# Performance work log

Hardware: AMD Instinct MI355X
Metric: run time of the kernel (lower is better)

## Reference

```python
import jax, jax.numpy as jnp
import numpy as np

P, B, H, IN, L = 64, 256, 512, 2, 2


def setup_inputs() -> dict:
    key = jax.random.key(0)
    ks = jax.random.split(key, 16)
    s = 1.0 / np.sqrt(H)
    inp = {
        'input_traces': jax.random.normal(ks[0], (B, P, IN), jnp.float32),
        'h0': jax.random.normal(ks[1], (P, L, B, H), jnp.float32) * 0.1,
        'c0': jax.random.normal(ks[2], (P, L, B, H), jnp.float32) * 0.1,
        # layer 0 LSTM params (PyTorch layout: [4H, in] with gate order i,f,g,o)
        'w_ih0': jax.random.uniform(ks[3], (4 * H, IN), jnp.float32, -s, s),
        'w_hh0': jax.random.uniform(ks[4], (4 * H, H), jnp.float32, -s, s),
        'b_ih0': jax.random.uniform(ks[5], (4 * H,), jnp.float32, -s, s),
        'b_hh0': jax.random.uniform(ks[6], (4 * H,), jnp.float32, -s, s),
        # layer 1 LSTM params
        'w_ih1': jax.random.uniform(ks[7], (4 * H, H), jnp.float32, -s, s),
        'w_hh1': jax.random.uniform(ks[8], (4 * H, H), jnp.float32, -s, s),
        'b_ih1': jax.random.uniform(ks[9], (4 * H,), jnp.float32, -s, s),
        'b_hh1': jax.random.uniform(ks[10], (4 * H,), jnp.float32, -s, s),
    }
    return inp


def _lstm_forward(input_traces, h0, c0, params):
    # Fuse pedestrian and batch dims into one big batch PB = P*B; the original
    # loops over pedestrians calling the SAME LSTM weights, so this is exact.
    x = jnp.transpose(input_traces, (1, 0, 2)).reshape(P * B, IN)  # [PB, 2]
    h = jnp.transpose(h0, (1, 0, 2, 3)).reshape(L, P * B, H)       # [L, PB, H]
    c = jnp.transpose(c0, (1, 0, 2, 3)).reshape(L, P * B, H)
    h_next, c_next = [], []
    for l in range(L):
        wi, wh, bi, bh = params[l]
        gates = x @ wi.T + bi + h[l] @ wh.T + bh                   # [PB, 4H]
        ig, fg, gg, og = jnp.split(gates, 4, axis=-1)
        ig, fg, og = jax.nn.sigmoid(ig), jax.nn.sigmoid(fg), jax.nn.sigmoid(og)
        gg = jnp.tanh(gg)
        c_new = fg * c[l] + ig * gg
        h_new = og * jnp.tanh(c_new)
        h_next.append(h_new)
        c_next.append(c_new)
        x = h_new
    out = x.reshape(P, B, H).transpose(1, 0, 2)                    # [B, P, H]
    hn = jnp.stack(h_next).reshape(L, P, B, H).transpose(1, 0, 2, 3)
    cn = jnp.stack(c_next).reshape(L, P, B, H).transpose(1, 0, 2, 3)
    return out, hn, cn


def reference(input_traces, h0, c0, w_ih0, w_hh0, b_ih0, b_hh0,
              w_ih1, w_hh1, b_ih1, b_hh1):
    params = [(w_ih0, w_hh0, b_ih0, b_hh0), (w_ih1, w_hh1, b_ih1, b_hh1)]
    return _lstm_forward(input_traces, h0, c0, params)
```

## Files before the change

kernel.cpp:

```cpp
#include <hip/hip_runtime.h>
#include <hip/hip_bf16.h>

#define PP 64
#define BB 256
#define HH 512
#define MM (PP * BB)

#define HN_BASE (BB * PP * HH)
#define CN_BASE (HN_BASE + PP * 2 * BB * HH)

#define TILE_BYTES 16384
#define WS_A0   0ull
#define WS_A1A  16777216ull
#define WS_A1B  33554432ull
#define WS_W0   50331648ull
#define WS_W1A  52428800ull
#define WS_W1B  54525952ull
#define WS_NEED 56623104ull

typedef __attribute__((ext_vector_type(8))) short bf16x8;
typedef __attribute__((ext_vector_type(4))) float floatx4;

__device__ __forceinline__ float sigf(float x) { return 1.0f / (1.0f + __expf(-x)); }
__device__ __forceinline__ float tanh_(float x) { return 2.0f / (1.0f + __expf(-2.0f * x)) - 1.0f; }

__device__ __forceinline__ short f2bf(float f) {
  unsigned u = __float_as_uint(f);
  u = (u + 0x7FFFu + ((u >> 16) & 1u)) >> 16;
  return (short)u;
}

template <typename T>
__device__ __forceinline__ float tofl(T v);
template <> __device__ __forceinline__ float tofl<float>(float v) { return v; }
template <> __device__ __forceinline__ float tofl<__hip_bfloat16>(__hip_bfloat16 v) { return __bfloat162float(v); }

template <typename T>
__device__ __forceinline__ T fromfl(float v);
template <> __device__ __forceinline__ float fromfl<float>(float v) { return v; }
template <> __device__ __forceinline__ __hip_bfloat16 fromfl<__hip_bfloat16>(float v) { return __float2bfloat16(v); }

template <typename T>
__device__ __forceinline__ bf16x8 load8(const T* p);
template <> __device__ __forceinline__ bf16x8 load8<__hip_bfloat16>(const __hip_bfloat16* p) {
  return *(const bf16x8*)p;
}
template <> __device__ __forceinline__ bf16x8 load8<float>(const float* p) {
  float4 f0 = *(const float4*)p;
  float4 f1 = *((const float4*)p + 1);
  bf16x8 v;
  v[0] = f2bf(f0.x); v[1] = f2bf(f0.y); v[2] = f2bf(f0.z); v[3] = f2bf(f0.w);
  v[4] = f2bf(f1.x); v[5] = f2bf(f1.y); v[6] = f2bf(f1.z); v[7] = f2bf(f1.w);
  return v;
}

__device__ __forceinline__ bool detect_f32(const void* w_ih0) {
  const unsigned short* p = (const unsigned short*)w_ih0;
  int l = threadIdx.x & 63;
  unsigned short a = p[2 * l], b = p[2 * l + 1];
  int big = ((a & 0x7F80) >= 0x3F80) || ((b & 0x7F80) >= 0x3F80);
  return __any(big);
}


template <typename T>
__device__ __forceinline__ void prep_A_body(const T* __restrict__ h0, char* __restrict__ ws) {
  const int pb = blockIdx.x, kt = blockIdx.y, l = blockIdx.z;
  char* dst = ws + (l ? WS_A1B : WS_A0) + ((size_t)(pb * 8 + kt)) * TILE_BYTES;
  const int ped = pb >> 1, bh = pb & 1;
  const T* src = h0 + ((size_t)(ped * 2 + l) * 256) * 512;
  const int tid = threadIdx.x;
#pragma unroll
  for (int i = 0; i < 4; ++i) {
    int idx = i * 256 + tid;
    int r = idx >> 3;
    int p = idx & 7;
    int c = p ^ (r & 7);
    *(bf16x8*)(dst + (size_t)idx * 16) =
        load8<T>(src + (size_t)(bh * 128 + r) * 512 + kt * 64 + c * 8);
  }
}

__global__ void __launch_bounds__(256) prep_A_k(const void* h0, const void* det, void* ws) {
  if (detect_f32(det)) prep_A_body<float>((const float*)h0, (char*)ws);
  else prep_A_body<__hip_bfloat16>((const __hip_bfloat16*)h0, (char*)ws);
}

template <typename T>
__device__ __forceinline__ void prep_W_body(const T* __restrict__ w0, const T* __restrict__ w1a,
                                            const T* __restrict__ w1b, char* __restrict__ ws) {
  const int m = blockIdx.x >> 4, hb = blockIdx.x & 15, kt = blockIdx.y;
  const T* src = (m == 0) ? w0 : (m == 1 ? w1a : w1b);
  const size_t base = (m == 0) ? WS_W0 : (m == 1 ? WS_W1A : WS_W1B);
  char* dst = ws + base + ((size_t)(hb * 8 + kt)) * TILE_BYTES;
  const int tid = threadIdx.x;
#pragma unroll
  for (int i = 0; i < 4; ++i) {
    int idx = i * 256 + tid;
    int r = idx >> 3;
    int p = idx & 7;
    int c = p ^ (r & 7);
    int j = (r >> 5) * 512 + hb * 32 + (r & 31);
    *(bf16x8*)(dst + (size_t)idx * 16) =
        load8<T>(src + (size_t)j * 512 + kt * 64 + c * 8);
  }
}

__global__ void __launch_bounds__(256) prep_W_k(const void* w0, const void* w1a, const void* w1b,
                                                const void* det, void* ws) {
  if (detect_f32(det)) prep_W_body<float>((const float*)w0, (const float*)w1a, (const float*)w1b, (char*)ws);
  else prep_W_body<__hip_bfloat16>((const __hip_bfloat16*)w0, (const __hip_bfloat16*)w1a,
                                   (const __hip_bfloat16*)w1b, (char*)ws);
}

template <typename T, int LAYER>
__device__ __forceinline__ void lstm_ws_body(
    const T* __restrict__ xin, const T* __restrict__ c0,
    const T* __restrict__ wih, const T* __restrict__ bih, const T* __restrict__ bhh,
    T* __restrict__ out, char* __restrict__ ws,
    char* __restrict__ ldsA, char* __restrict__ ldsW)
{
  const int tid  = threadIdx.x;
  const int nb   = blockIdx.x;
  const int hb   = blockIdx.y;
  const int lane = tid & 63;
  const int wid  = tid >> 6;
  const int quad = lane >> 4;
  const int lrow = lane & 15;
  const int p0   = nb >> 1;

  floatx4 acc[4][4];
#pragma unroll
  for (int g = 0; g < 4; ++g)
#pragma unroll
    for (int mi = 0; mi < 4; ++mi)
#pragma unroll
      for (int q = 0; q < 4; ++q) acc[g][mi][q] = 0.0f;

  int arow[4], wrow[4];
#pragma unroll
  for (int mi = 0; mi < 4; ++mi) arow[mi] = (wid >> 1) * 64 + mi * 16 + lrow;
#pragma unroll
  for (int g = 0; g < 4; ++g) wrow[g] = g * 32 + (wid & 1) * 16 + lrow;

  constexpr int KITERS = (LAYER == 0) ? 8 : 16;

  auto tileptr = [&](int kt, const char*& at, const char*& wt) {
    if (LAYER == 0) {
      at = ws + WS_A0  + ((size_t)(nb * 8 + kt)) * TILE_BYTES;
      wt = ws + WS_W0  + ((size_t)(hb * 8 + kt)) * TILE_BYTES;
    } else if (kt < 8) {
      at = ws + WS_A1A + ((size_t)(nb * 8 + kt)) * TILE_BYTES;
      wt = ws + WS_W1A + ((size_t)(hb * 8 + kt)) * TILE_BYTES;
    } else {
      at = ws + WS_A1B + ((size_t)(nb * 8 + kt - 8)) * TILE_BYTES;
      wt = ws + WS_W1B + ((size_t)(hb * 8 + kt - 8)) * TILE_BYTES;
    }
  };

  bf16x8 rA[4], rW[4];
  {
    const char *at, *wt;
    tileptr(0, at, wt);
#pragma unroll
    for (int i = 0; i < 4; ++i) {
      int off = (i * 256 + tid) * 16;
      rA[i] = *(const bf16x8*)(at + off);
      rW[i] = *(const bf16x8*)(wt + off);
    }
  }

  for (int kt = 0; kt < KITERS; ++kt) {
    __syncthreads();
#pragma unroll
    for (int i = 0; i < 4; ++i) {
      int off = (i * 256 + tid) * 16;
      *(bf16x8*)(ldsA + off) = rA[i];
      *(bf16x8*)(ldsW + off) = rW[i];
    }
    __syncthreads();

    if (kt + 1 < KITERS) {
      const char *at, *wt;
      tileptr(kt + 1, at, wt);
#pragma unroll
      for (int i = 0; i < 4; ++i) {
        int off = (i * 256 + tid) * 16;
        rA[i] = *(const bf16x8*)(at + off);
        rW[i] = *(const bf16x8*)(wt + off);
      }
    }

#pragma unroll
    for (int ks = 0; ks < 2; ++ks) {
      bf16x8 aF[4], wF[4];
#pragma unroll
      for (int mi = 0; mi < 4; ++mi) {
        int ch = (ks * 4 + quad) ^ (arow[mi] & 7);
        aF[mi] = *(const bf16x8*)(ldsA + arow[mi] * 128 + ch * 16);
      }
#pragma unroll
      for (int g = 0; g < 4; ++g) {
        int ch = (ks * 4 + quad) ^ (wrow[g] & 7);
        wF[g] = *(const bf16x8*)(ldsW + wrow[g] * 128 + ch * 16);
      }
#pragma unroll
      for (int g = 0; g < 4; ++g)
#pragma unroll
        for (int mi = 0; mi < 4; ++mi)
          acc[g][mi] = __builtin_amdgcn_mfma_f32_16x16x32_bf16(
              aF[mi], wF[g], acc[g][mi], 0, 0, 0);
    }
  }

  const int hloc = hb * 32 + (wid & 1) * 16 + lrow;
  float bias[4], wx0[4], wx1[4];
#pragma unroll
  for (int g = 0; g < 4; ++g) {
    int j = g * 512 + hloc;
    bias[g] = tofl<T>(bih[j]) + tofl<T>(bhh[j]);
    if (LAYER == 0) {
      wx0[g] = tofl<T>(wih[j * 2]);
      wx1[g] = tofl<T>(wih[j * 2 + 1]);
    }
  }
  const int crow0 = (p0 * 2 + LAYER) * 256;
  const int kt_h = hloc >> 6;
  const int cl   = (hloc >> 3) & 7;
  const int wib  = hloc & 7;
  char* a1a_tile = ws + WS_A1A + ((size_t)(nb * 8 + kt_h)) * TILE_BYTES;

#pragma unroll
  for (int mi = 0; mi < 4; ++mi) {
#pragma unroll
    for (int r = 0; r < 4; ++r) {
      int rr = (wid >> 1) * 64 + mi * 16 + quad * 4 + r;
      int b  = ((nb & 1) << 7) + rr;
      float gv0 = acc[0][mi][r] + bias[0];
      float gv1 = acc[1][mi][r] + bias[1];
      float gv2 = acc[2][mi][r] + bias[2];
      float gv3 = acc[3][mi][r] + bias[3];
      if (LAYER == 0) {
        float x0 = tofl<T>(xin[(b * 64 + p0) * 2]);
        float x1 = tofl<T>(xin[(b * 64 + p0) * 2 + 1]);
        gv0 += x0 * wx0[0] + x1 * wx1[0];
        gv1 += x0 * wx0[1] + x1 * wx1[1];
        gv2 += x0 * wx0[2] + x1 * wx1[2];
        gv3 += x0 * wx0[3] + x1 * wx1[3];
      }
      float ig = sigf(gv0), fg = sigf(gv1);
      float gg = tanh_(gv2), og = sigf(gv3);
      size_t ro = ((size_t)(crow0 + b)) * 512 + hloc;
      float co   = tofl<T>(c0[ro]);
      float cnew = fg * co + ig * gg;
      float hnew = og * tanh_(cnew);
      out[HN_BASE + ro] = fromfl<T>(hnew);
      out[CN_BASE + ro] = fromfl<T>(cnew);
      if (LAYER == 0) {
        *(short*)(a1a_tile + rr * 128 + ((cl ^ (rr & 7)) * 16) + wib * 2) = f2bf(hnew);
      }
      if (LAYER == 1)
        out[(size_t)(b * 64 + p0) * 512 + hloc] = fromfl<T>(hnew);
    }
  }
}

template <int LAYER>
__global__ void __launch_bounds__(256)
lstm_ws(const void* xin, const void* c0, const void* wih,
        const void* bih, const void* bhh, const void* det,
        void* out, void* ws)
{
  __shared__ __align__(16) char ldsA[TILE_BYTES];
  __shared__ __align__(16) char ldsW[TILE_BYTES];
  if (detect_f32(det)) {
    lstm_ws_body<float, LAYER>((const float*)xin, (const float*)c0, (const float*)wih,
                               (const float*)bih, (const float*)bhh,
                               (float*)out, (char*)ws, ldsA, ldsW);
  } else {
    lstm_ws_body<__hip_bfloat16, LAYER>((const __hip_bfloat16*)xin, (const __hip_bfloat16*)c0,
                                        (const __hip_bfloat16*)wih, (const __hip_bfloat16*)bih,
                                        (const __hip_bfloat16*)bhh,
                                        (__hip_bfloat16*)out, (char*)ws, ldsA, ldsW);
  }
}

template <typename T, int LAYER>
__device__ __forceinline__ void lstm_body(
    const T* __restrict__ xin, const T* __restrict__ h0, const T* __restrict__ c0,
    const T* __restrict__ wih, const T* __restrict__ whh,
    const T* __restrict__ bih, const T* __restrict__ bhh,
    T* out, __hip_bfloat16* ldsA, __hip_bfloat16* ldsW)
{
  const int tid  = threadIdx.x;
  const int nb   = blockIdx.x;
  const int hb   = blockIdx.y;
  const int lane = tid & 63;
  const int wid  = tid >> 6;
  const int quad = lane >> 4;
  const int lrow = lane & 15;
  const int p0   = nb >> 1;

  floatx4 acc[4][4];
#pragma unroll
  for (int g = 0; g < 4; ++g)
#pragma unroll
    for (int mi = 0; mi < 4; ++mi)
#pragma unroll
      for (int q = 0; q < 4; ++q) acc[g][mi][q] = 0.0f;

  int arow[4], wrow[4];
#pragma unroll
  for (int mi = 0; mi < 4; ++mi) arow[mi] = (wid >> 1) * 64 + mi * 16 + lrow;
#pragma unroll
  for (int g = 0; g < 4; ++g) wrow[g] = g * 32 + (wid & 1) * 16 + lrow;

  const int sr = tid >> 3;
  const int sc = tid & 7;
  const int KITERS = (LAYER == 0) ? 8 : 16;

  for (int kt = 0; kt < KITERS; ++kt) {
    bf16x8 ra[4], rw[4];
#pragma unroll
    for (int round = 0; round < 4; ++round) {
      int r = sr + round * 32;
      int b = ((nb & 1) << 7) + r;
      const T* srcA;
      if (LAYER == 0) {
        srcA = h0 + ((size_t)((p0 * 2) * 256 + b)) * 512 + kt * 64 + sc * 8;
      } else {
        if (kt < 8)
          srcA = out + HN_BASE + ((size_t)((p0 * 2) * 256 + b)) * 512 + kt * 64 + sc * 8;
        else
          srcA = h0 + ((size_t)((p0 * 2 + 1) * 256 + b)) * 512 + (kt - 8) * 64 + sc * 8;
      }
      ra[round] = load8<T>(srcA);

      int j = (r >> 5) * 512 + hb * 32 + (r & 31);
      const T* srcW;
      if (LAYER == 0) {
        srcW = whh + (size_t)j * 512 + kt * 64 + sc * 8;
      } else {
        if (kt < 8) srcW = wih + (size_t)j * 512 + kt * 64 + sc * 8;
        else        srcW = whh + (size_t)j * 512 + (kt - 8) * 64 + sc * 8;
      }
      rw[round] = load8<T>(srcW);
    }

    __syncthreads();
#pragma unroll
    for (int round = 0; round < 4; ++round) {
      int r = sr + round * 32;
      int p = sc ^ (r & 7);
      *(bf16x8*)((char*)ldsA + r * 128 + p * 16) = ra[round];
      *(bf16x8*)((char*)ldsW + r * 128 + p * 16) = rw[round];
    }
    __syncthreads();

#pragma unroll
    for (int ks = 0; ks < 2; ++ks) {
      bf16x8 aF[4], wF[4];
#pragma unroll
      for (int mi = 0; mi < 4; ++mi) {
        int ch = (ks * 4 + quad) ^ (arow[mi] & 7);
        aF[mi] = *(const bf16x8*)((const char*)ldsA + arow[mi] * 128 + ch * 16);
      }
#pragma unroll
      for (int g = 0; g < 4; ++g) {
        int ch = (ks * 4 + quad) ^ (wrow[g] & 7);
        wF[g] = *(const bf16x8*)((const char*)ldsW + wrow[g] * 128 + ch * 16);
      }
#pragma unroll
      for (int g = 0; g < 4; ++g)
#pragma unroll
        for (int mi = 0; mi < 4; ++mi)
          acc[g][mi] = __builtin_amdgcn_mfma_f32_16x16x32_bf16(
              aF[mi], wF[g], acc[g][mi], 0, 0, 0);
    }
  }

  const int hloc = hb * 32 + (wid & 1) * 16 + lrow;
  float bias[4], wx0[4], wx1[4];
#pragma unroll
  for (int g = 0; g < 4; ++g) {
    int j = g * 512 + hloc;
    bias[g] = tofl<T>(bih[j]) + tofl<T>(bhh[j]);
    if (LAYER == 0) {
      wx0[g] = tofl<T>(wih[j * 2]);
      wx1[g] = tofl<T>(wih[j * 2 + 1]);
    }
  }
  const int crow0 = (p0 * 2 + LAYER) * 256;
#pragma unroll
  for (int mi = 0; mi < 4; ++mi) {
#pragma unroll
    for (int r = 0; r < 4; ++r) {
      int b = ((nb & 1) << 7) + (wid >> 1) * 64 + mi * 16 + quad * 4 + r;
      float gv0 = acc[0][mi][r] + bias[0];
      float gv1 = acc[1][mi][r] + bias[1];
      float gv2 = acc[2][mi][r] + bias[2];
      float gv3 = acc[3][mi][r] + bias[3];
      if (LAYER == 0) {
        float x0 = tofl<T>(xin[(b * 64 + p0) * 2]);
        float x1 = tofl<T>(xin[(b * 64 + p0) * 2 + 1]);
        gv0 += x0 * wx0[0] + x1 * wx1[0];
        gv1 += x0 * wx0[1] + x1 * wx1[1];
        gv2 += x0 * wx0[2] + x1 * wx1[2];
        gv3 += x0 * wx0[3] + x1 * wx1[3];
      }
      float ig = sigf(gv0), fg = sigf(gv1);
      float gg = tanh_(gv2), og = sigf(gv3);
      size_t ro = ((size_t)(crow0 + b)) * 512 + hloc;
      float co   = tofl<T>(c0[ro]);
      float cnew = fg * co + ig * gg;
      float hnew = og * tanh_(cnew);
      out[HN_BASE + ro] = fromfl<T>(hnew);
      out[CN_BASE + ro] = fromfl<T>(cnew);
      if (LAYER == 1)
        out[(size_t)(b * 64 + p0) * 512 + hloc] = fromfl<T>(hnew);
    }
  }
}

template <int LAYER>
__global__ void __launch_bounds__(256)
lstm_layer(const void* xin, const void* h0, const void* c0,
           const void* wih, const void* whh, const void* bih, const void* bhh,
           const void* w_ih0_detect, void* out)
{
  __shared__ __align__(16) __hip_bfloat16 ldsA[128 * 64];
  __shared__ __align__(16) __hip_bfloat16 ldsW[128 * 64];
  if (detect_f32(w_ih0_detect)) {
    lstm_body<float, LAYER>((const float*)xin, (const float*)h0, (const float*)c0,
                            (const float*)wih, (const float*)whh,
                            (const float*)bih, (const float*)bhh,
                            (float*)out, ldsA, ldsW);
  } else {
    lstm_body<__hip_bfloat16, LAYER>((const __hip_bfloat16*)xin, (const __hip_bfloat16*)h0,
                                     (const __hip_bfloat16*)c0, (const __hip_bfloat16*)wih,
                                     (const __hip_bfloat16*)whh, (const __hip_bfloat16*)bih,
                                     (const __hip_bfloat16*)bhh, (__hip_bfloat16*)out,
                                     ldsA, ldsW);
  }
}

extern "C" void kernel_launch(void* const* d_in, const int* in_sizes, int n_in,
                              void* d_out, int out_size, void* d_ws, size_t ws_size,
                              hipStream_t stream) {
  dim3 block(256);
  if (d_ws != nullptr && ws_size >= WS_NEED) {
    prep_A_k<<<dim3(128, 8, 2), block, 0, stream>>>(d_in[1], d_in[3], d_ws);
    prep_W_k<<<dim3(48, 8), block, 0, stream>>>(d_in[4], d_in[7], d_in[8], d_in[3], d_ws);
    dim3 grid(MM / 128, HH / 32);
    lstm_ws<0><<<grid, block, 0, stream>>>(d_in[0], d_in[2], d_in[3],
                                           d_in[5], d_in[6], d_in[3], d_out, d_ws);
    lstm_ws<1><<<grid, block, 0, stream>>>(d_in[0], d_in[2], d_in[3],
                                           d_in[9], d_in[10], d_in[3], d_out, d_ws);
  } else {
    dim3 grid(MM / 128, HH / 32);
    lstm_layer<0><<<grid, block, 0, stream>>>(d_in[0], d_in[1], d_in[2],
                                              d_in[3], d_in[4], d_in[5], d_in[6],
                                              d_in[3], d_out);
    lstm_layer<1><<<grid, block, 0, stream>>>(d_in[0], d_in[1], d_in[2],
                                              d_in[7], d_in[8], d_in[9], d_in[10],
                                              d_in[3], d_out);
  }
}
```

Measured before the change: 500.2 us.

## Pre-swizzle workspace into MFMA fragment order and drop LDS staging

Measured after the change: 573.8 us. 14.7% more time.

```diff
diff --git a/kernel.cpp b/kernel.cpp
--- a/kernel.cpp
+++ b/kernel.cpp
@@ -73,11 +73,12 @@
 #pragma unroll
   for (int i = 0; i < 4; ++i) {
     int idx = i * 256 + tid;
-    int r = idx >> 3;
-    int p = idx & 7;
-    int c = p ^ (r & 7);
-    *(bf16x8*)(dst + (size_t)idx * 16) =
-        load8<T>(src + (size_t)(bh * 128 + r) * 512 + kt * 64 + c * 8);
+    int ln  = idx & 63;
+    int ks  = (idx >> 6) & 1;
+    int rb  = idx >> 7;
+    int row = bh * 128 + rb * 16 + (ln & 15);
+    int col = kt * 64 + ks * 32 + (ln >> 4) * 8;
+    *(bf16x8*)(dst + (size_t)idx * 16) = load8<T>(src + (size_t)row * 512 + col);
   }
 }
 
@@ -97,12 +98,13 @@
 #pragma unroll
   for (int i = 0; i < 4; ++i) {
     int idx = i * 256 + tid;
-    int r = idx >> 3;
-    int p = idx & 7;
-    int c = p ^ (r & 7);
-    int j = (r >> 5) * 512 + hb * 32 + (r & 31);
-    *(bf16x8*)(dst + (size_t)idx * 16) =
-        load8<T>(src + (size_t)j * 512 + kt * 64 + c * 8);
+    int ln  = idx & 63;
+    int ks  = (idx >> 6) & 1;
+    int rb  = idx >> 7;
+    int g   = rb >> 1, half = rb & 1;
+    int j   = g * 512 + hb * 32 + half * 16 + (ln & 15);
+    int col = kt * 64 + ks * 32 + (ln >> 4) * 8;
+    *(bf16x8*)(dst + (size_t)idx * 16) = load8<T>(src + (size_t)j * 512 + col);
   }
 }
 
@@ -114,11 +116,10 @@
 }
 
 template <typename T, int LAYER>
-__device__ __forceinline__ void lstm_ws_body(
+__device__ __forceinline__ void lstm_frag_body(
     const T* __restrict__ xin, const T* __restrict__ c0,
     const T* __restrict__ wih, const T* __restrict__ bih, const T* __restrict__ bhh,
-    T* __restrict__ out, char* __restrict__ ws,
-    char* __restrict__ ldsA, char* __restrict__ ldsW)
+    T* __restrict__ out, char* __restrict__ ws)
 {
   const int tid  = threadIdx.x;
   const int nb   = blockIdx.x;
@@ -137,15 +138,14 @@
 #pragma unroll
       for (int q = 0; q < 4; ++q) acc[g][mi][q] = 0.0f;
 
-  int arow[4], wrow[4];
-#pragma unroll
-  for (int mi = 0; mi < 4; ++mi) arow[mi] = (wid >> 1) * 64 + mi * 16 + lrow;
-#pragma unroll
-  for (int g = 0; g < 4; ++g) wrow[g] = g * 32 + (wid & 1) * 16 + lrow;
+  const int a_rb0  = (wid >> 1) * 4;
+  const int w_half = wid & 1;
 
   constexpr int KITERS = (LAYER == 0) ? 8 : 16;
 
-  auto tileptr = [&](int kt, const char*& at, const char*& wt) {
+#pragma unroll
+  for (int kt = 0; kt < KITERS; ++kt) {
+    const char *at, *wt;
     if (LAYER == 0) {
       at = ws + WS_A0  + ((size_t)(nb * 8 + kt)) * TILE_BYTES;
       wt = ws + WS_W0  + ((size_t)(hb * 8 + kt)) * TILE_BYTES;
@@ -156,54 +156,15 @@
       at = ws + WS_A1B + ((size_t)(nb * 8 + kt - 8)) * TILE_BYTES;
       wt = ws + WS_W1B + ((size_t)(hb * 8 + kt - 8)) * TILE_BYTES;
     }
-  };
-
-  bf16x8 rA[4], rW[4];
-  {
-    const char *at, *wt;
-    tileptr(0, at, wt);
-#pragma unroll
-    for (int i = 0; i < 4; ++i) {
-      int off = (i * 256 + tid) * 16;
-      rA[i] = *(const bf16x8*)(at + off);
-      rW[i] = *(const bf16x8*)(wt + off);
-    }
-  }
-
-  for (int kt = 0; kt < KITERS; ++kt) {
-    __syncthreads();
-#pragma unroll
-    for (int i = 0; i < 4; ++i) {
-      int off = (i * 256 + tid) * 16;
-      *(bf16x8*)(ldsA + off) = rA[i];
-      *(bf16x8*)(ldsW + off) = rW[i];
-    }
-    __syncthreads();
-
-    if (kt + 1 < KITERS) {
-      const char *at, *wt;
-      tileptr(kt + 1, at, wt);
-#pragma unroll
-      for (int i = 0; i < 4; ++i) {
-        int off = (i * 256 + tid) * 16;
-        rA[i] = *(const bf16x8*)(at + off);
-        rW[i] = *(const bf16x8*)(wt + off);
-      }
-    }
-
 #pragma unroll
     for (int ks = 0; ks < 2; ++ks) {
       bf16x8 aF[4], wF[4];
 #pragma unroll
-      for (int mi = 0; mi < 4; ++mi) {
-        int ch = (ks * 4 + quad) ^ (arow[mi] & 7);
-        aF[mi] = *(const bf16x8*)(ldsA + arow[mi] * 128 + ch * 16);
-      }
-#pragma unroll
-      for (int g = 0; g < 4; ++g) {
-        int ch = (ks * 4 + quad) ^ (wrow[g] & 7);
-        wF[g] = *(const bf16x8*)(ldsW + wrow[g] * 128 + ch * 16);
-      }
+      for (int mi = 0; mi < 4; ++mi)
+        aF[mi] = *(const bf16x8*)(at + (((a_rb0 + mi) * 2 + ks) * 1024) + lane * 16);
+#pragma unroll
+      for (int g = 0; g < 4; ++g)
+        wF[g] = *(const bf16x8*)(wt + (((g * 2 + w_half) * 2 + ks) * 1024) + lane * 16);
 #pragma unroll
       for (int g = 0; g < 4; ++g)
 #pragma unroll
@@ -213,7 +174,7 @@
     }
   }
 
-  const int hloc = hb * 32 + (wid & 1) * 16 + lrow;
+  const int hloc = hb * 32 + w_half * 16 + lrow;
   float bias[4], wx0[4], wx1[4];
 #pragma unroll
   for (int g = 0; g < 4; ++g) {
@@ -226,8 +187,9 @@
   }
   const int crow0 = (p0 * 2 + LAYER) * 256;
   const int kt_h = hloc >> 6;
-  const int cl   = (hloc >> 3) & 7;
-  const int wib  = hloc & 7;
+  const int ks_h = (hloc >> 5) & 1;
+  const int qd_h = (hloc >> 3) & 3;
+  const int el_h = hloc & 7;
   char* a1a_tile = ws + WS_A1A + ((size_t)(nb * 8 + kt_h)) * TILE_BYTES;
 
 #pragma unroll
@@ -257,7 +219,8 @@
       out[HN_BASE + ro] = fromfl<T>(hnew);
       out[CN_BASE + ro] = fromfl<T>(cnew);
       if (LAYER == 0) {
-        *(short*)(a1a_tile + rr * 128 + ((cl ^ (rr & 7)) * 16) + wib * 2) = f2bf(hnew);
+        int slot = (((rr >> 4) * 2 + ks_h) * 64) + qd_h * 16 + (rr & 15);
+        *(short*)(a1a_tile + (size_t)slot * 16 + el_h * 2) = f2bf(hnew);
       }
       if (LAYER == 1)
         out[(size_t)(b * 64 + p0) * 512 + hloc] = fromfl<T>(hnew);
@@ -266,22 +229,20 @@
 }
 
 template <int LAYER>
-__global__ void __launch_bounds__(256)
-lstm_ws(const void* xin, const void* c0, const void* wih,
-        const void* bih, const void* bhh, const void* det,
-        void* out, void* ws)
+__global__ void __launch_bounds__(256, 3)
+lstm_frag(const void* xin, const void* c0, const void* wih,
+          const void* bih, const void* bhh, const void* det,
+          void* out, void* ws)
 {
-  __shared__ __align__(16) char ldsA[TILE_BYTES];
-  __shared__ __align__(16) char ldsW[TILE_BYTES];
   if (detect_f32(det)) {
-    lstm_ws_body<float, LAYER>((const float*)xin, (const float*)c0, (const float*)wih,
-                               (const float*)bih, (const float*)bhh,
-                               (float*)out, (char*)ws, ldsA, ldsW);
+    lstm_frag_body<float, LAYER>((const float*)xin, (const float*)c0, (const float*)wih,
+                                 (const float*)bih, (const float*)bhh,
+                                 (float*)out, (char*)ws);
   } else {
-    lstm_ws_body<__hip_bfloat16, LAYER>((const __hip_bfloat16*)xin, (const __hip_bfloat16*)c0,
-                                        (const __hip_bfloat16*)wih, (const __hip_bfloat16*)bih,
-                                        (const __hip_bfloat16*)bhh,
-                                        (__hip_bfloat16*)out, (char*)ws, ldsA, ldsW);
+    lstm_frag_body<__hip_bfloat16, LAYER>((const __hip_bfloat16*)xin, (const __hip_bfloat16*)c0,
+                                          (const __hip_bfloat16*)wih, (const __hip_bfloat16*)bih,
+                                          (const __hip_bfloat16*)bhh,
+                                          (__hip_bfloat16*)out, (char*)ws);
   }
 }
 
@@ -452,10 +413,10 @@
     prep_A_k<<<dim3(128, 8, 2), block, 0, stream>>>(d_in[1], d_in[3], d_ws);
     prep_W_k<<<dim3(48, 8), block, 0, stream>>>(d_in[4], d_in[7], d_in[8], d_in[3], d_ws);
     dim3 grid(MM / 128, HH / 32);
-    lstm_ws<0><<<grid, block, 0, stream>>>(d_in[0], d_in[2], d_in[3],
-                                           d_in[5], d_in[6], d_in[3], d_out, d_ws);
-    lstm_ws<1><<<grid, block, 0, stream>>>(d_in[0], d_in[2], d_in[3],
-                                           d_in[9], d_in[10], d_in[3], d_out, d_ws);
+    lstm_frag<0><<<grid, block, 0, stream>>>(d_in[0], d_in[2], d_in[3],
+                                             d_in[5], d_in[6], d_in[3], d_out, d_ws);
+    lstm_frag<1><<<grid, block, 0, stream>>>(d_in[0], d_in[2], d_in[3],
+                                             d_in[9], d_in[10], d_in[3], d_out, d_ws);
   } else {
     dim3 grid(MM / 128, HH / 32);
     lstm_layer<0><<<grid, block, 0, stream>>>(d_in[0], d_in[1], d_in[2],
```
